# Kernel optimization log

Measured on AMD Instinct MI355X. Metric: run time of the kernel, lower is better.

Reference implementation:

```python
import jax, jax.numpy as jnp
import numpy as np

B, N, D, H = 4, 2048, 512, 8
HD = D // H


def setup_inputs() -> dict:
    key = jax.random.key(0)
    ks = jax.random.split(key, 10)
    x = jax.random.normal(ks[0], (B, N, D), dtype=jnp.float32)
    adj = (jax.random.uniform(ks[1], (N, N)) < 0.1).astype(jnp.float32)
    s = 1.0 / np.sqrt(D)
    Wq = jax.random.normal(ks[2], (D, D), dtype=jnp.float32) * s
    Wk = jax.random.normal(ks[3], (D, D), dtype=jnp.float32) * s
    Wv = jax.random.normal(ks[4], (D, D), dtype=jnp.float32) * s
    Wo = jax.random.normal(ks[5], (D, D), dtype=jnp.float32) * s
    bq = jnp.zeros((D,), jnp.float32)
    bk = jnp.zeros((D,), jnp.float32)
    bv = jnp.zeros((D,), jnp.float32)
    bo = jnp.zeros((D,), jnp.float32)
    return {"x": x, "adj": adj, "Wq": Wq, "bq": bq, "Wk": Wk, "bk": bk,
            "Wv": Wv, "bv": bv, "Wo": Wo, "bo": bo}


def reference(x, adj, Wq, bq, Wk, bk, Wv, bv, Wo, bo):
    b, n, d = x.shape
    q = (x @ Wq + bq).reshape(b, n, H, HD)
    k = (x @ Wk + bk).reshape(b, n, H, HD)
    v = (x @ Wv + bv).reshape(b, n, H, HD)
    scores = jnp.einsum('bqhd,bkhd->bhqk', q, k) / jnp.sqrt(jnp.float32(HD))
    scores = scores + (1.0 - adj)[None, None, :, :] * (-1e9)
    attn = jax.nn.softmax(scores, axis=-1)
    out = jnp.einsum('bhqk,bkhd->bqhd', attn, v).reshape(b, n, d)
    return out @ Wo + bo
```

## Files before the change

kernel.cpp:

```cpp
#include <hip/hip_runtime.h>
#include <math.h>

#define NB    4
#define NSEQ  2048
#define DMODEL 512
#define NH    8
#define HDIM  64
#define STR   72
#define LOG2E 1.44269504088896f

typedef __attribute__((ext_vector_type(8))) short short8;
typedef __attribute__((ext_vector_type(4))) float f32x4;
typedef __attribute__((ext_vector_type(16))) float f32x16;
typedef __attribute__((ext_vector_type(2))) unsigned int uint2v;
#define MFMA16 __builtin_amdgcn_mfma_f32_16x16x32_bf16
#define MFMA32 __builtin_amdgcn_mfma_f32_32x32x16_bf16
#define EXP2F __builtin_amdgcn_exp2f

__device__ __forceinline__ unsigned short f2bf(float f) {
    union { float f; unsigned int u; } v; v.f = f;
    unsigned int u = v.u;
    unsigned int r = (u + 0x7FFFu + ((u >> 16) & 1u)) >> 16;
    return (unsigned short)r;
}
__device__ __forceinline__ void async16(void* lds, const void* g) {
    __builtin_amdgcn_global_load_lds(
        (const __attribute__((address_space(1))) unsigned int*)g,
        (__attribute__((address_space(3))) unsigned int*)lds, 16, 0, 0);
}
__device__ __forceinline__ unsigned cvtpk(float lo, float hi) {
    unsigned r;
    asm("v_cvt_pk_bf16_f32 %0, %1, %2" : "=v"(r) : "v"(lo), "v"(hi));
    return r;
}
__device__ __forceinline__ void pswap(unsigned& a, unsigned& b) {
    uint2v r = __builtin_amdgcn_permlane32_swap(a, b, false, false);
    a = r[0]; b = r[1];
}

__global__ __launch_bounds__(256) void prep_kernel(
    const float* __restrict__ adj, unsigned long long* __restrict__ Mb,
    const float* __restrict__ x, unsigned short* __restrict__ xhi,
    const float* __restrict__ Wq, const float* __restrict__ Wk,
    const float* __restrict__ Wv, const float* __restrict__ Wo,
    unsigned short* __restrict__ Wthi)
{
    __shared__ float tile[32][33];
    const int bid = blockIdx.x;
    if (bid < 16384) {
        const int w    = bid * 4 + (threadIdx.x >> 6);
        const int lane = threadIdx.x & 63;
        const int q  = w >> 5;
        const int kt = w & 31;
        float a = adj[(size_t)q * NSEQ + kt * 64 + lane];
        unsigned long long m = __ballot(a > 0.5f);
        if (lane == 0) Mb[(size_t)kt * NSEQ + q] = m;
    } else if (bid < 20480) {
        const int gid = (bid - 16384) * 256 + threadIdx.x;
        float4 a = ((const float4*)x)[gid];
        ushort4 h4;
        h4.x = f2bf(a.x); h4.y = f2bf(a.y); h4.z = f2bf(a.z); h4.w = f2bf(a.w);
        ((ushort4*)xhi)[gid] = h4;
    } else {
        const int local = bid - 20480;
        const int m  = local >> 8;
        const int rem = local & 255;
        const int k0 = (rem & 15) * 32, n0 = (rem >> 4) * 32;
        const float* W = (m == 0) ? Wq : (m == 1) ? Wk : (m == 2) ? Wv : Wo;
        const int tx = threadIdx.x & 31, ty = threadIdx.x >> 5;
        #pragma unroll
        for (int i = 0; i < 4; ++i)
            tile[ty * 4 + i][tx] = W[(size_t)(k0 + ty * 4 + i) * DMODEL + n0 + tx];
        __syncthreads();
        const size_t base = ((size_t)m * DMODEL) * DMODEL;
        #pragma unroll
        for (int i = 0; i < 4; ++i) {
            float f = tile[tx][ty * 4 + i];
            size_t idx = base + (size_t)(n0 + ty * 4 + i) * DMODEL + k0 + tx;
            Wthi[idx] = f2bf(f);
        }
    }
}

__device__ __forceinline__ void gemm_k_loop(
    const unsigned short* __restrict__ Ah,
    const unsigned short* __restrict__ Bh,
    char* smem, f32x4 acc[4][4])
{
    const int t    = threadIdx.x;
    const int lane = t & 63;
    const int wid  = t >> 6;
    const int quad = lane >> 4, l16 = lane & 15;
    const int wm   = wid >> 1,  wn  = wid & 1;

    const int ci0 = t, ci1 = 256 + t;
    const int r0 = ci0 >> 2, r1 = ci1 >> 2;
    const int c0 = (ci0 & 3) ^ ((r0 >> 1) & 3);
    const int c1 = (ci1 & 3) ^ ((r1 >> 1) & 3);
    const char* gAh = (const char*)Ah;
    const char* gBh = (const char*)Bh;
    const int ca = quad ^ ((l16 >> 1) & 3);

    for (int k0 = 0; k0 < DMODEL; k0 += 64) {
        #pragma unroll
        for (int hf = 0; hf < 2; ++hf) {
            char* base  = smem + hf * 16384;
            const int kb = (k0 + hf * 32) * 2;
            async16(base + ci0 * 16,        gAh + r0 * 1024 + kb + c0 * 16);
            async16(base + ci1 * 16,        gAh + r1 * 1024 + kb + c1 * 16);
            async16(base + 8192 + ci0 * 16, gBh + r0 * 1024 + kb + c0 * 16);
            async16(base + 8192 + ci1 * 16, gBh + r1 * 1024 + kb + c1 * 16);
        }
        __syncthreads();

        #pragma unroll
        for (int hf = 0; hf < 2; ++hf) {
            unsigned short* As_h = (unsigned short*)(smem + hf * 16384);
            unsigned short* Bs_h = (unsigned short*)(smem + hf * 16384 + 8192);
            short8 ah[4], bh[4];
            #pragma unroll
            for (int i = 0; i < 4; ++i) {
                const int Ra = wm * 64 + i * 16 + l16;
                ah[i] = *(const short8*)(As_h + Ra * 32 + ca * 8);
                const int Rb = wn * 64 + i * 16 + l16;
                bh[i] = *(const short8*)(Bs_h + Rb * 32 + ca * 8);
            }
            #pragma unroll
            for (int mi = 0; mi < 4; ++mi)
                #pragma unroll
                for (int ni = 0; ni < 4; ++ni)
                    acc[mi][ni] = MFMA16(ah[mi], bh[ni], acc[mi][ni], 0, 0, 0);
        }
        __syncthreads();
    }
}

__global__ __launch_bounds__(256, 4) void qkv_mfma_kernel(
    const unsigned short* __restrict__ xhi,
    const unsigned short* __restrict__ Wthi,
    const float* __restrict__ bq, const float* __restrict__ bk, const float* __restrict__ bv,
    unsigned short* __restrict__ Qhi,
    unsigned short* __restrict__ Khi,
    unsigned short* __restrict__ Vt)
{
    __shared__ __align__(16) char smem[33280];
    const int t    = threadIdx.x;
    const int lane = t & 63;
    const int wid  = t >> 6;
    const int quad = lane >> 4, l16 = lane & 15;
    const int wm   = wid >> 1,  wn  = wid & 1;

    const int f    = blockIdx.x + 64 * blockIdx.y;
    const int xcd  = f & 7;
    const int loc  = f >> 3;
    const int row0 = (xcd * 8 + (loc & 7)) * 128;
    const int yb   = loc >> 3;
    const int mtx  = yb >> 2;
    const int col0 = (yb & 3) * 128;

    f32x4 acc[4][4];
    #pragma unroll
    for (int i = 0; i < 4; ++i)
        #pragma unroll
        for (int j = 0; j < 4; ++j) acc[i][j] = (f32x4){0.f, 0.f, 0.f, 0.f};

    const size_t wslot = (size_t)mtx * DMODEL * DMODEL;
    gemm_k_loop(xhi + (size_t)row0 * DMODEL,
                Wthi + wslot + (size_t)col0 * DMODEL, smem, acc);

    const float* bias = (mtx == 0) ? bq : (mtx == 1) ? bk : bv;
    float bcol[4];
    #pragma unroll
    for (int ni = 0; ni < 4; ++ni) bcol[ni] = bias[col0 + wn * 64 + ni * 16 + l16];
    const int h = (col0 + wn * 64) >> 6;

    if (mtx < 2) {
        const float scale = (mtx == 0) ? (0.125f * LOG2E) : 1.0f;
        unsigned short* hig = (mtx == 0) ? Qhi : Khi;
        #pragma unroll
        for (int mi = 0; mi < 4; ++mi) {
            #pragma unroll
            for (int reg = 0; reg < 4; ++reg) {
                const int r = row0 + wm * 64 + mi * 16 + quad * 4 + reg;
                const int b = r >> 11, n = r & 2047;
                const size_t rowbase = ((size_t)(b * NH + h) * NSEQ + n) * HDIM;
                #pragma unroll
                for (int ni = 0; ni < 4; ++ni)
                    hig[rowbase + ni * 16 + l16] =
                        f2bf((acc[mi][ni][reg] + bcol[ni]) * scale);
            }
        }
    } else {
        __syncthreads();
        unsigned short* vt = (unsigned short*)smem + (size_t)wid * 64 * 65;
        #pragma unroll
        for (int mi = 0; mi < 4; ++mi)
            #pragma unroll
            for (int ni = 0; ni < 4; ++ni)
                #pragma unroll
                for (int reg = 0; reg < 4; ++reg)
                    vt[(mi * 16 + quad * 4 + reg) * 65 + ni * 16 + l16] =
                        f2bf(acc[mi][ni][reg] + bcol[ni]);
        const int b   = row0 >> 11;
        const int n0g = (row0 & 2047) + wm * 64;
        const int bh  = b * NH + h;
        unsigned short* gdst = Vt + ((size_t)bh * HDIM + lane) * NSEQ + n0g;
        #pragma unroll
        for (int nb = 0; nb < 8; ++nb) {
            unsigned short v[8];
            #pragma unroll
            for (int j = 0; j < 8; ++j) v[j] = vt[(nb * 8 + j) * 65 + lane];
            uint4 u;
            u.x = (unsigned)v[0] | ((unsigned)v[1] << 16);
            u.y = (unsigned)v[2] | ((unsigned)v[3] << 16);
            u.z = (unsigned)v[4] | ((unsigned)v[5] << 16);
            u.w = (unsigned)v[6] | ((unsigned)v[7] << 16);
            *(uint4*)(gdst + nb * 8) = u;
        }
    }
}

__global__ __launch_bounds__(256, 4) void out_mfma_kernel(
    const unsigned short* __restrict__ chi,
    const unsigned short* __restrict__ Wthi,
    const float* __restrict__ bo, float* __restrict__ out)
{
    __shared__ __align__(16) char smem[32768];
    const int t    = threadIdx.x;
    const int lane = t & 63;
    const int wid  = t >> 6;
    const int quad = lane >> 4, l16 = lane & 15;
    const int wm   = wid >> 1,  wn  = wid & 1;

    const int f    = blockIdx.x + 64 * blockIdx.y;
    const int xcd  = f & 7;
    const int loc  = f >> 3;
    const int row0 = (xcd * 8 + (loc & 7)) * 128;
    const int col0 = (loc >> 3) * 128;

    f32x4 acc[4][4];
    #pragma unroll
    for (int i = 0; i < 4; ++i)
        #pragma unroll
        for (int j = 0; j < 4; ++j) acc[i][j] = (f32x4){0.f, 0.f, 0.f, 0.f};

    const size_t wslot = (size_t)3 * DMODEL * DMODEL;
    gemm_k_loop(chi + (size_t)row0 * DMODEL,
                Wthi + wslot + (size_t)col0 * DMODEL, smem, acc);

    float bcol[4];
    #pragma unroll
    for (int ni = 0; ni < 4; ++ni) bcol[ni] = bo[col0 + wn * 64 + ni * 16 + l16];
    #pragma unroll
    for (int mi = 0; mi < 4; ++mi)
        #pragma unroll
        for (int reg = 0; reg < 4; ++reg) {
            const int r = row0 + wm * 64 + mi * 16 + quad * 4 + reg;
            float* orow = out + (size_t)r * DMODEL + col0 + wn * 64 + l16;
            #pragma unroll
            for (int ni = 0; ni < 4; ++ni)
                orow[ni * 16] = acc[mi][ni][reg] + bcol[ni];
        }
}

__global__ __launch_bounds__(256, 4) void attn_kernel(
    const unsigned short* __restrict__ Qhi,
    const unsigned short* __restrict__ Khi,
    const unsigned short* __restrict__ Vt,
    const unsigned long long* __restrict__ Mb,
    unsigned short* __restrict__ Opart, float* __restrict__ lpart,
    const int split, const int sshift)
{
    __shared__ __align__(16) unsigned short KS[64 * STR];
    __shared__ __align__(16) unsigned short VS[64 * STR];
    __shared__ unsigned long long mlut[16];

    const int t    = threadIdx.x;
    const int wq   = t >> 6;
    const int lane = t & 63;
    const int l32  = lane & 31;
    const int hw   = lane >> 5;

    const int flat = blockIdx.x + 16 * (blockIdx.y + 8 * blockIdx.z);
    const int xcd  = flat & 7;
    const int u    = flat >> 3;
    const int zi   = xcd * (split >> 1) + (u >> 7);
    const int h    = u & 7;
    const int qt   = (u >> 3) & 15;
    const int b    = zi >> sshift;
    const int ks   = zi & (split - 1);
    const int ktSpan = 32 >> sshift;
    const int bh   = b * NH + h;
    const int qa   = qt * 128 + wq * 32;

    if (t < 16) {
        unsigned long long m = 0;
        if (t & 1) m |= 0xFFFFull;
        if (t & 2) m |= 0xFFFF0000ull;
        if (t & 4) m |= 0xFFFFull << 32;
        if (t & 8) m |= 0xFFFFull << 48;
        mlut[t] = m;
    }

    short8 qh[4];
    #pragma unroll
    for (int s = 0; s < 4; ++s)
        qh[s] = *(const short8*)(Qhi + ((size_t)bh * NSEQ + qa + l32) * HDIM + s * 16 + hw * 8);
    const unsigned long long* mrow = Mb + (qa + l32);

    short8 onesf;
    #pragma unroll
    for (int i = 0; i < 8; ++i) onesf[i] = (short)0x3F80;

    f32x16 O0, O1, Ol;
    #pragma unroll
    for (int i = 0; i < 16; ++i) { O0[i] = 0.f; O1[i] = 0.f; Ol[i] = 0.f; }

    const unsigned short* gk = Khi + (size_t)bh * NSEQ * HDIM;
    const unsigned short* gv = Vt  + (size_t)bh * HDIM * NSEQ;

    const int ci0 = t, ci1 = t + 256;
    const int sr0 = ci0 >> 3, sc0 = (ci0 & 7) * 8;
    const int sr1 = ci1 >> 3, sc1 = (ci1 & 7) * 8;

    const int ktBeg = ks * ktSpan, ktEnd = ktBeg + ktSpan;

    {
        const int k0 = ktBeg * 64;
        uint4 ka = *(const uint4*)(gk + (size_t)(k0 + sr0) * HDIM + sc0);
        uint4 kc = *(const uint4*)(gk + (size_t)(k0 + sr1) * HDIM + sc1);
        uint4 va = *(const uint4*)(gv + (size_t)sr0 * NSEQ + k0 + sc0);
        uint4 vc = *(const uint4*)(gv + (size_t)sr1 * NSEQ + k0 + sc1);
        *(uint4*)&KS[sr0 * STR + sc0] = ka;
        *(uint4*)&KS[sr1 * STR + sc1] = kc;
        *(uint4*)&VS[sr0 * STR + sc0] = va;
        *(uint4*)&VS[sr1 * STR + sc1] = vc;
    }
    __syncthreads();

    for (int kt = ktBeg; kt < ktEnd; ++kt) {
        const unsigned short* ksrc = KS;
        const unsigned short* vsrc = VS;
        const unsigned long long mw = mrow[(size_t)kt * NSEQ];

        short8 pf[4];
        #pragma unroll
        for (int nt = 0; nt < 2; ++nt) {
            f32x16 S;
            #pragma unroll
            for (int i = 0; i < 16; ++i) S[i] = 0.f;
            __builtin_amdgcn_s_setprio(1);
            #pragma unroll
            for (int s = 0; s < 4; ++s) {
                short8 kb = *(const short8*)&ksrc[(nt * 32 + l32) * STR + s * 16 + hw * 8];
                S = MFMA32(kb, qh[s], S, 0, 0, 0);
            }
            __builtin_amdgcn_s_setprio(0);
            float p[16];
            #pragma unroll
            for (int r = 0; r < 16; ++r) p[r] = EXP2F(S[r]);
            unsigned w[8];
            #pragma unroll
            for (int i = 0; i < 8; ++i) w[i] = cvtpk(p[2 * i], p[2 * i + 1]);
            pswap(w[0], w[2]); pswap(w[1], w[3]);
            pswap(w[4], w[6]); pswap(w[5], w[7]);
            union { short8 s8; unsigned u[4]; } A, B2;
            A.u[0] = w[0]; A.u[1] = w[1]; A.u[2] = w[2]; A.u[3] = w[3];
            B2.u[0] = w[4]; B2.u[1] = w[5]; B2.u[2] = w[6]; B2.u[3] = w[7];
            pf[2 * nt]     = A.s8;
            pf[2 * nt + 1] = B2.s8;
        }

        uint4 nk0, nk1, nv0, nv1;
        const bool more = (kt + 1 < ktEnd);
        if (more) {
            const int k0n = (kt + 1) * 64;
            nk0 = *(const uint4*)(gk + (size_t)(k0n + sr0) * HDIM + sc0);
            nk1 = *(const uint4*)(gk + (size_t)(k0n + sr1) * HDIM + sc1);
            nv0 = *(const uint4*)(gv + (size_t)sr0 * NSEQ + k0n + sc0);
            nv1 = *(const uint4*)(gv + (size_t)sr1 * NSEQ + k0n + sc1);
        }

        #pragma unroll
        for (int s = 0; s < 4; ++s) {
            const unsigned bits8 = (unsigned)(mw >> (s * 16 + hw * 8)) & 0xFFu;
            const unsigned long long lo = mlut[bits8 & 15u];
            const unsigned long long hi = mlut[bits8 >> 4];
            union { short8 s8; uint4 u; } x; x.s8 = pf[s];
            x.u.x &= (unsigned)lo; x.u.y &= (unsigned)(lo >> 32);
            x.u.z &= (unsigned)hi; x.u.w &= (unsigned)(hi >> 32);
            pf[s] = x.s8;
        }

        __builtin_amdgcn_s_setprio(1);
        #pragma unroll
        for (int s = 0; s < 4; ++s) {
            short8 v0 = *(const short8*)&vsrc[(l32) * STR + s * 16 + hw * 8];
            short8 v1 = *(const short8*)&vsrc[(32 + l32) * STR + s * 16 + hw * 8];
            O0 = MFMA32(pf[s], v0, O0, 0, 0, 0);
            O1 = MFMA32(pf[s], v1, O1, 0, 0, 0);
            Ol = MFMA32(pf[s], onesf, Ol, 0, 0, 0);
        }
        __builtin_amdgcn_s_setprio(0);

        __syncthreads();
        if (more) {
            *(uint4*)&KS[sr0 * STR + sc0] = nk0;
            *(uint4*)&KS[sr1 * STR + sc1] = nk1;
            *(uint4*)&VS[sr0 * STR + sc0] = nv0;
            *(uint4*)&VS[sr1 * STR + sc1] = nv1;
        }
        __syncthreads();
    }

    const size_t obase = ((size_t)(ks * NB + b) * NH + h) * NSEQ;
    #pragma unroll
    for (int r = 0; r < 16; ++r) {
        const int qrow = qa + (r & 3) + 8 * (r >> 2) + 4 * hw;
        unsigned short* orow = Opart + (obase + qrow) * HDIM;
        orow[l32]      = f2bf(O0[r]);
        orow[32 + l32] = f2bf(O1[r]);
        if (l32 == 0) lpart[obase + qrow] = Ol[r];
    }
}

__global__ __launch_bounds__(256) void merge_kernel(
    const unsigned short* __restrict__ Opart, const float* __restrict__ lpart,
    unsigned short* __restrict__ chi, const int split)
{
    const int g = blockIdx.x * 256 + threadIdx.x;
    const int qitem = g >> 2;
    const int grp = g & 3;
    const size_t QS = (size_t)NB * NH * NSEQ;
    const size_t HS = QS * HDIM;

    float lsum = 0.f;
    for (int i = 0; i < split; ++i) lsum += lpart[qitem + (size_t)i * QS];
    const float inv = 1.0f / lsum;

    float acc[16];
    #pragma unroll
    for (int j = 0; j < 16; ++j) acc[j] = 0.f;
    const unsigned short* pa = Opart + (size_t)qitem * HDIM + grp * 16;
    for (int i = 0; i < split; ++i) {
        const unsigned short* p = pa + (size_t)i * HS;
        uint4 v0 = *(const uint4*)(p);
        uint4 v1 = *(const uint4*)(p + 8);
        const unsigned wv[8] = {v0.x, v0.y, v0.z, v0.w, v1.x, v1.y, v1.z, v1.w};
        #pragma unroll
        for (int j = 0; j < 8; ++j) {
            union { unsigned u; float f; } lo, hi;
            lo.u = wv[j] << 16;
            hi.u = wv[j] & 0xFFFF0000u;
            acc[2 * j]     += lo.f;
            acc[2 * j + 1] += hi.f;
        }
    }

    const int n = qitem & 2047, h = (qitem >> 11) & 7, b = qitem >> 14;
    unsigned short* dst = chi + ((size_t)b * NSEQ + n) * DMODEL + h * HDIM + grp * 16;

    unsigned short o[16];
    #pragma unroll
    for (int j = 0; j < 16; ++j) o[j] = f2bf(acc[j] * inv);
    uint4 u0, u1;
    u0.x = (unsigned)o[0]  | ((unsigned)o[1]  << 16);
    u0.y = (unsigned)o[2]  | ((unsigned)o[3]  << 16);
    u0.z = (unsigned)o[4]  | ((unsigned)o[5]  << 16);
    u0.w = (unsigned)o[6]  | ((unsigned)o[7]  << 16);
    u1.x = (unsigned)o[8]  | ((unsigned)o[9]  << 16);
    u1.y = (unsigned)o[10] | ((unsigned)o[11] << 16);
    u1.z = (unsigned)o[12] | ((unsigned)o[13] << 16);
    u1.w = (unsigned)o[14] | ((unsigned)o[15] << 16);
    *(uint4*)dst = u0;
    *(uint4*)(dst + 8) = u1;
}

extern "C" void kernel_launch(void* const* d_in, const int* in_sizes, int n_in,
                              void* d_out, int out_size, void* d_ws, size_t ws_size,
                              hipStream_t stream) {
    const float* x   = (const float*)d_in[0];
    const float* adj = (const float*)d_in[1];
    const float* Wq  = (const float*)d_in[2];
    const float* bq  = (const float*)d_in[3];
    const float* Wk  = (const float*)d_in[4];
    const float* bk  = (const float*)d_in[5];
    const float* Wv  = (const float*)d_in[6];
    const float* bv  = (const float*)d_in[7];
    const float* Wo  = (const float*)d_in[8];
    const float* bo  = (const float*)d_in[9];
    float* out = (float*)d_out;

    const size_t elems = (size_t)NB * NSEQ * DMODEL;
    unsigned short* Qhi  = (unsigned short*)d_ws;
    unsigned short* Khi  = Qhi + elems;
    unsigned short* Vt   = Khi + elems;
    unsigned long long* Mbits = (unsigned long long*)(Vt + elems);
    unsigned short* xhi  = (unsigned short*)(Mbits + 32 * NSEQ);
    unsigned short* Wthi = xhi + elems;
    unsigned short* Opart = Wthi + 4 * (size_t)DMODEL * DMODEL;
    unsigned short* chi = xhi;

    const size_t QS = (size_t)NB * NH * NSEQ;
    const size_t head = (size_t)((char*)Opart - (char*)d_ws);
    const size_t per_split = QS * HDIM * 2 + QS * 4;
    const int split  = (ws_size >= head + 4 * per_split) ? 4 : 2;
    const int sshift = (split == 4) ? 2 : 1;
    float* lpart = (float*)(Opart + (size_t)split * QS * HDIM);

    prep_kernel<<<dim3(21504), dim3(256), 0, stream>>>(
        adj, Mbits, x, xhi, Wq, Wk, Wv, Wo, Wthi);
    qkv_mfma_kernel<<<dim3(64, 12), dim3(256), 0, stream>>>(
        xhi, Wthi, bq, bk, bv, Qhi, Khi, Vt);
    attn_kernel<<<dim3(NSEQ / 128, NH, NB * split), dim3(256), 0, stream>>>(
        Qhi, Khi, Vt, Mbits, Opart, lpart, split, sshift);
    merge_kernel<<<dim3(1024), dim3(256), 0, stream>>>(Opart, lpart, chi, split);
    out_mfma_kernel<<<dim3(64, 4), dim3(256), 0, stream>>>(
        chi, Wthi, bo, out);
}
```

Measured before the change: 185.9 us.

## Fuse split-K attention merge into output projection GEMM A-tile load

Removes the separate merge kernel and instead reduces the split attention partials (sum of partial outputs divided by the summed normalizers) while staging the A tile of the output projection GEMM into LDS. This drops one launch and the round trip of the merged bf16 context buffer through global memory. In exchange, each of the four column blocks repeats the merge work and the partial reads for its rows. The A-tile loads are now synchronous register loads rather than async LDS copies, which may reduce overlap in the GEMM loop.

```diff
diff --git a/kernel.cpp b/kernel.cpp
--- a/kernel.cpp
+++ b/kernel.cpp
@@ -22,6 +22,10 @@
     unsigned int u = v.u;
     unsigned int r = (u + 0x7FFFu + ((u >> 16) & 1u)) >> 16;
     return (unsigned short)r;
+}
+__device__ __forceinline__ float bf2f(unsigned short h) {
+    union { unsigned int u; float f; } v; v.u = (unsigned)h << 16;
+    return v.f;
 }
 __device__ __forceinline__ void async16(void* lds, const void* g) {
     __builtin_amdgcn_global_load_lds(
@@ -220,10 +224,35 @@
     }
 }
 
+__device__ __forceinline__ void merge_chunk(
+    unsigned short* dst, const unsigned short* __restrict__ Opart,
+    size_t ob, float inv, int split)
+{
+    const size_t QSH = (size_t)NB * NH * NSEQ * HDIM;
+    float s0 = 0, s1 = 0, s2 = 0, s3 = 0, s4 = 0, s5 = 0, s6 = 0, s7 = 0;
+    #pragma unroll
+    for (int i = 0; i < 4; ++i) {
+        if (i < split) {
+            uint4 v = *(const uint4*)(Opart + (size_t)i * QSH + ob);
+            s0 += bf2f((unsigned short)v.x);  s1 += bf2f((unsigned short)(v.x >> 16));
+            s2 += bf2f((unsigned short)v.y);  s3 += bf2f((unsigned short)(v.y >> 16));
+            s4 += bf2f((unsigned short)v.z);  s5 += bf2f((unsigned short)(v.z >> 16));
+            s6 += bf2f((unsigned short)v.w);  s7 += bf2f((unsigned short)(v.w >> 16));
+        }
+    }
+    uint4 o;
+    o.x = cvtpk(s0 * inv, s1 * inv);
+    o.y = cvtpk(s2 * inv, s3 * inv);
+    o.z = cvtpk(s4 * inv, s5 * inv);
+    o.w = cvtpk(s6 * inv, s7 * inv);
+    *(uint4*)dst = o;
+}
+
 __global__ __launch_bounds__(256, 4) void out_mfma_kernel(
-    const unsigned short* __restrict__ chi,
+    const unsigned short* __restrict__ Opart, const float* __restrict__ lpart,
     const unsigned short* __restrict__ Wthi,
-    const float* __restrict__ bo, float* __restrict__ out)
+    const float* __restrict__ bo, float* __restrict__ out,
+    const int split)
 {
     __shared__ __align__(16) char smem[32768];
     const int t    = threadIdx.x;
@@ -238,15 +267,71 @@
     const int row0 = (xcd * 8 + (loc & 7)) * 128;
     const int col0 = (loc >> 3) * 128;
 
+    const size_t QS = (size_t)NB * NH * NSEQ;
+
     f32x4 acc[4][4];
     #pragma unroll
     for (int i = 0; i < 4; ++i)
         #pragma unroll
         for (int j = 0; j < 4; ++j) acc[i][j] = (f32x4){0.f, 0.f, 0.f, 0.f};
 
-    const size_t wslot = (size_t)3 * DMODEL * DMODEL;
-    gemm_k_loop(chi + (size_t)row0 * DMODEL,
-                Wthi + wslot + (size_t)col0 * DMODEL, smem, acc);
+    const int ci0 = t, ci1 = 256 + t;
+    const int r0 = ci0 >> 2, r1 = ci1 >> 2;
+    const int c0 = (ci0 & 3) ^ ((r0 >> 1) & 3);
+    const int c1 = (ci1 & 3) ^ ((r1 >> 1) & 3);
+    const char* gBh = (const char*)(Wthi + (size_t)3 * DMODEL * DMODEL
+                                    + (size_t)col0 * DMODEL);
+    const int ca = quad ^ ((l16 >> 1) & 3);
+
+    const int grow0 = row0 + r0, grow1 = row0 + r1;
+    const int qb0 = (grow0 >> 11) * NH * NSEQ + (grow0 & 2047);
+    const int qb1 = (grow1 >> 11) * NH * NSEQ + (grow1 & 2047);
+
+    for (int k0 = 0; k0 < DMODEL; k0 += 64) {
+        const int hN = (k0 >> 6) * NSEQ;
+        float ls0 = 0.f, ls1 = 0.f;
+        #pragma unroll
+        for (int i = 0; i < 4; ++i) {
+            if (i < split) {
+                ls0 += lpart[(size_t)i * QS + qb0 + hN];
+                ls1 += lpart[(size_t)i * QS + qb1 + hN];
+            }
+        }
+        const float inv0 = 1.0f / ls0, inv1 = 1.0f / ls1;
+
+        #pragma unroll
+        for (int hf = 0; hf < 2; ++hf) {
+            char* base  = smem + hf * 16384;
+            const int kb = (k0 + hf * 32) * 2;
+            async16(base + 8192 + ci0 * 16, gBh + r0 * 1024 + kb + c0 * 16);
+            async16(base + 8192 + ci1 * 16, gBh + r1 * 1024 + kb + c1 * 16);
+            merge_chunk((unsigned short*)base + ci0 * 8, Opart,
+                        ((size_t)(qb0 + hN)) * HDIM + hf * 32 + c0 * 8, inv0, split);
+            merge_chunk((unsigned short*)base + ci1 * 8, Opart,
+                        ((size_t)(qb1 + hN)) * HDIM + hf * 32 + c1 * 8, inv1, split);
+        }
+        __syncthreads();
+
+        #pragma unroll
+        for (int hf = 0; hf < 2; ++hf) {
+            unsigned short* As_h = (unsigned short*)(smem + hf * 16384);
+            unsigned short* Bs_h = (unsigned short*)(smem + hf * 16384 + 8192);
+            short8 ah[4], bh[4];
+            #pragma unroll
+            for (int i = 0; i < 4; ++i) {
+                const int Ra = wm * 64 + i * 16 + l16;
+                ah[i] = *(const short8*)(As_h + Ra * 32 + ca * 8);
+                const int Rb = wn * 64 + i * 16 + l16;
+                bh[i] = *(const short8*)(Bs_h + Rb * 32 + ca * 8);
+            }
+            #pragma unroll
+            for (int mi = 0; mi < 4; ++mi)
+                #pragma unroll
+                for (int ni = 0; ni < 4; ++ni)
+                    acc[mi][ni] = MFMA16(ah[mi], bh[ni], acc[mi][ni], 0, 0, 0);
+        }
+        __syncthreads();
+    }
 
     float bcol[4];
     #pragma unroll
@@ -422,58 +507,6 @@
         orow[32 + l32] = f2bf(O1[r]);
         if (l32 == 0) lpart[obase + qrow] = Ol[r];
     }
-}
-
-__global__ __launch_bounds__(256) void merge_kernel(
-    const unsigned short* __restrict__ Opart, const float* __restrict__ lpart,
-    unsigned short* __restrict__ chi, const int split)
-{
-    const int g = blockIdx.x * 256 + threadIdx.x;
-    const int qitem = g >> 2;
-    const int grp = g & 3;
-    const size_t QS = (size_t)NB * NH * NSEQ;
-    const size_t HS = QS * HDIM;
-
-    float lsum = 0.f;
-    for (int i = 0; i < split; ++i) lsum += lpart[qitem + (size_t)i * QS];
-    const float inv = 1.0f / lsum;
-
-    float acc[16];
-    #pragma unroll
-    for (int j = 0; j < 16; ++j) acc[j] = 0.f;
-    const unsigned short* pa = Opart + (size_t)qitem * HDIM + grp * 16;
-    for (int i = 0; i < split; ++i) {
-        const unsigned short* p = pa + (size_t)i * HS;
-        uint4 v0 = *(const uint4*)(p);
-        uint4 v1 = *(const uint4*)(p + 8);
-        const unsigned wv[8] = {v0.x, v0.y, v0.z, v0.w, v1.x, v1.y, v1.z, v1.w};
-        #pragma unroll
-        for (int j = 0; j < 8; ++j) {
-            union { unsigned u; float f; } lo, hi;
-            lo.u = wv[j] << 16;
-            hi.u = wv[j] & 0xFFFF0000u;
-            acc[2 * j]     += lo.f;
-            acc[2 * j + 1] += hi.f;
-        }
-    }
-
-    const int n = qitem & 2047, h = (qitem >> 11) & 7, b = qitem >> 14;
-    unsigned short* dst = chi + ((size_t)b * NSEQ + n) * DMODEL + h * HDIM + grp * 16;
-
-    unsigned short o[16];
-    #pragma unroll
-    for (int j = 0; j < 16; ++j) o[j] = f2bf(acc[j] * inv);
-    uint4 u0, u1;
-    u0.x = (unsigned)o[0]  | ((unsigned)o[1]  << 16);
-    u0.y = (unsigned)o[2]  | ((unsigned)o[3]  << 16);
-    u0.z = (unsigned)o[4]  | ((unsigned)o[5]  << 16);
-    u0.w = (unsigned)o[6]  | ((unsigned)o[7]  << 16);
-    u1.x = (unsigned)o[8]  | ((unsigned)o[9]  << 16);
-    u1.y = (unsigned)o[10] | ((unsigned)o[11] << 16);
-    u1.z = (unsigned)o[12] | ((unsigned)o[13] << 16);
-    u1.w = (unsigned)o[14] | ((unsigned)o[15] << 16);
-    *(uint4*)dst = u0;
-    *(uint4*)(dst + 8) = u1;
 }
 
 extern "C" void kernel_launch(void* const* d_in, const int* in_sizes, int n_in,
@@ -499,7 +532,6 @@
     unsigned short* xhi  = (unsigned short*)(Mbits + 32 * NSEQ);
     unsigned short* Wthi = xhi + elems;
     unsigned short* Opart = Wthi + 4 * (size_t)DMODEL * DMODEL;
-    unsigned short* chi = xhi;
 
     const size_t QS = (size_t)NB * NH * NSEQ;
     const size_t head = (size_t)((char*)Opart - (char*)d_ws);
@@ -514,7 +546,6 @@
         xhi, Wthi, bq, bk, bv, Qhi, Khi, Vt);
     attn_kernel<<<dim3(NSEQ / 128, NH, NB * split), dim3(256), 0, stream>>>(
         Qhi, Khi, Vt, Mbits, Opart, lpart, split, sshift);
-    merge_kernel<<<dim3(1024), dim3(256), 0, stream>>>(Opart, lpart, chi, split);
     out_mfma_kernel<<<dim3(64, 4), dim3(256), 0, stream>>>(
-        chi, Wthi, bo, out);
-}
+        Opart, lpart, Wthi, bo, out, split);
+}
```

After: 207.9 us. +11.8%, slower.

## Fuse split-K merge into attention kernel via last-block atomic counter

Applied to the files above, without the earlier changes.

Removes the separate merge kernel launch. Each attention block now increments a per-(batch,head,q-tile) atomic counter, and the last arriving split block sums the partial O and l values and writes the normalized bf16 output into chi. This saves one kernel launch and its drain/ramp gap, and reads the partials while they are likely still in cache. In exchange it adds a memset, threadfences, and a serialized tail of work in the last block of each tile.

```diff
diff --git a/kernel.cpp b/kernel.cpp
--- a/kernel.cpp
+++ b/kernel.cpp
@@ -22,6 +22,10 @@
     unsigned int u = v.u;
     unsigned int r = (u + 0x7FFFu + ((u >> 16) & 1u)) >> 16;
     return (unsigned short)r;
+}
+__device__ __forceinline__ float bf2f(unsigned short h) {
+    union { unsigned int u; float f; } v; v.u = (unsigned)h << 16;
+    return v.f;
 }
 __device__ __forceinline__ void async16(void* lds, const void* g) {
     __builtin_amdgcn_global_load_lds(
@@ -269,11 +273,13 @@
     const unsigned short* __restrict__ Vt,
     const unsigned long long* __restrict__ Mb,
     unsigned short* __restrict__ Opart, float* __restrict__ lpart,
+    unsigned short* __restrict__ chi, int* __restrict__ cnt,
     const int split, const int sshift)
 {
     __shared__ __align__(16) unsigned short KS[64 * STR];
     __shared__ __align__(16) unsigned short VS[64 * STR];
     __shared__ unsigned long long mlut[16];
+    __shared__ int done;
 
     const int t    = threadIdx.x;
     const int wq   = t >> 6;
@@ -422,58 +428,55 @@
         orow[32 + l32] = f2bf(O1[r]);
         if (l32 == 0) lpart[obase + qrow] = Ol[r];
     }
-}
-
-__global__ __launch_bounds__(256) void merge_kernel(
-    const unsigned short* __restrict__ Opart, const float* __restrict__ lpart,
-    unsigned short* __restrict__ chi, const int split)
-{
-    const int g = blockIdx.x * 256 + threadIdx.x;
-    const int qitem = g >> 2;
-    const int grp = g & 3;
-    const size_t QS = (size_t)NB * NH * NSEQ;
-    const size_t HS = QS * HDIM;
-
-    float lsum = 0.f;
-    for (int i = 0; i < split; ++i) lsum += lpart[qitem + (size_t)i * QS];
-    const float inv = 1.0f / lsum;
-
-    float acc[16];
-    #pragma unroll
-    for (int j = 0; j < 16; ++j) acc[j] = 0.f;
-    const unsigned short* pa = Opart + (size_t)qitem * HDIM + grp * 16;
-    for (int i = 0; i < split; ++i) {
-        const unsigned short* p = pa + (size_t)i * HS;
-        uint4 v0 = *(const uint4*)(p);
-        uint4 v1 = *(const uint4*)(p + 8);
-        const unsigned wv[8] = {v0.x, v0.y, v0.z, v0.w, v1.x, v1.y, v1.z, v1.w};
-        #pragma unroll
-        for (int j = 0; j < 8; ++j) {
-            union { unsigned u; float f; } lo, hi;
-            lo.u = wv[j] << 16;
-            hi.u = wv[j] & 0xFFFF0000u;
-            acc[2 * j]     += lo.f;
-            acc[2 * j + 1] += hi.f;
-        }
-    }
-
-    const int n = qitem & 2047, h = (qitem >> 11) & 7, b = qitem >> 14;
-    unsigned short* dst = chi + ((size_t)b * NSEQ + n) * DMODEL + h * HDIM + grp * 16;
-
-    unsigned short o[16];
-    #pragma unroll
-    for (int j = 0; j < 16; ++j) o[j] = f2bf(acc[j] * inv);
-    uint4 u0, u1;
-    u0.x = (unsigned)o[0]  | ((unsigned)o[1]  << 16);
-    u0.y = (unsigned)o[2]  | ((unsigned)o[3]  << 16);
-    u0.z = (unsigned)o[4]  | ((unsigned)o[5]  << 16);
-    u0.w = (unsigned)o[6]  | ((unsigned)o[7]  << 16);
-    u1.x = (unsigned)o[8]  | ((unsigned)o[9]  << 16);
-    u1.y = (unsigned)o[10] | ((unsigned)o[11] << 16);
-    u1.z = (unsigned)o[12] | ((unsigned)o[13] << 16);
-    u1.w = (unsigned)o[14] | ((unsigned)o[15] << 16);
-    *(uint4*)dst = u0;
-    *(uint4*)(dst + 8) = u1;
+
+    __threadfence();
+    __syncthreads();
+    if (t == 0) done = atomicAdd(&cnt[(bh << 4) + qt], 1);
+    __syncthreads();
+    if (done == split - 1) {
+        __threadfence();
+        const size_t QS = (size_t)NB * NH * NSEQ;
+        const int r  = t >> 1;
+        const int dh = (t & 1) * 32;
+        const int n  = qt * 128 + r;
+        const size_t rowoff = (size_t)bh * NSEQ + n;
+        float ls = 0.f;
+        #pragma unroll
+        for (int i = 0; i < 4; ++i)
+            if (i < split) ls += lpart[(size_t)i * QS + rowoff];
+        const float inv = 1.0f / ls;
+        float av[32];
+        #pragma unroll
+        for (int j = 0; j < 32; ++j) av[j] = 0.f;
+        #pragma unroll
+        for (int i = 0; i < 4; ++i) {
+            if (i < split) {
+                const unsigned short* p = Opart + ((size_t)i * QS + rowoff) * HDIM + dh;
+                #pragma unroll
+                for (int c = 0; c < 4; ++c) {
+                    uint4 v = *(const uint4*)(p + c * 8);
+                    av[c*8+0] += bf2f((unsigned short)v.x);
+                    av[c*8+1] += bf2f((unsigned short)(v.x >> 16));
+                    av[c*8+2] += bf2f((unsigned short)v.y);
+                    av[c*8+3] += bf2f((unsigned short)(v.y >> 16));
+                    av[c*8+4] += bf2f((unsigned short)v.z);
+                    av[c*8+5] += bf2f((unsigned short)(v.z >> 16));
+                    av[c*8+6] += bf2f((unsigned short)v.w);
+                    av[c*8+7] += bf2f((unsigned short)(v.w >> 16));
+                }
+            }
+        }
+        unsigned short* dst = chi + ((size_t)b * NSEQ + n) * DMODEL + h * HDIM + dh;
+        #pragma unroll
+        for (int c = 0; c < 4; ++c) {
+            uint4 o;
+            o.x = cvtpk(av[c*8+0] * inv, av[c*8+1] * inv);
+            o.y = cvtpk(av[c*8+2] * inv, av[c*8+3] * inv);
+            o.z = cvtpk(av[c*8+4] * inv, av[c*8+5] * inv);
+            o.w = cvtpk(av[c*8+6] * inv, av[c*8+7] * inv);
+            *(uint4*)(dst + c * 8) = o;
+        }
+    }
 }
 
 extern "C" void kernel_launch(void* const* d_in, const int* in_sizes, int n_in,
@@ -504,17 +507,18 @@
     const size_t QS = (size_t)NB * NH * NSEQ;
     const size_t head = (size_t)((char*)Opart - (char*)d_ws);
     const size_t per_split = QS * HDIM * 2 + QS * 4;
-    const int split  = (ws_size >= head + 4 * per_split) ? 4 : 2;
+    const int split  = (ws_size >= head + 4 * per_split + 4096) ? 4 : 2;
     const int sshift = (split == 4) ? 2 : 1;
     float* lpart = (float*)(Opart + (size_t)split * QS * HDIM);
-
+    int* cnt = (int*)((char*)lpart + (size_t)split * QS * sizeof(float));
+
+    hipMemsetAsync(cnt, 0, 512 * sizeof(int), stream);
     prep_kernel<<<dim3(21504), dim3(256), 0, stream>>>(
         adj, Mbits, x, xhi, Wq, Wk, Wv, Wo, Wthi);
     qkv_mfma_kernel<<<dim3(64, 12), dim3(256), 0, stream>>>(
         xhi, Wthi, bq, bk, bv, Qhi, Khi, Vt);
     attn_kernel<<<dim3(NSEQ / 128, NH, NB * split), dim3(256), 0, stream>>>(
-        Qhi, Khi, Vt, Mbits, Opart, lpart, split, sshift);
-    merge_kernel<<<dim3(1024), dim3(256), 0, stream>>>(Opart, lpart, chi, split);
+        Qhi, Khi, Vt, Mbits, Opart, lpart, chi, cnt, split, sshift);
     out_mfma_kernel<<<dim3(64, 4), dim3(256), 0, stream>>>(
         chi, Wthi, bo, out);
 }
```

New measurement: 537.9 us. +189.4%, slower.
